# Kernel optimization log

Measured on AMD Instinct MI355X. Metric: run time of the kernel, lower is better.

## Reference

```python
import jax, jax.numpy as jnp
import numpy as np

B, S = 64, 1000
ENC, DEC = 512, 512


def setup_inputs() -> dict:
    key = jax.random.key(0)
    k1, k2, k3, k4, k5 = jax.random.split(key, 5)
    hidden = jax.random.normal(k1, (B, DEC), dtype=jnp.float32)
    encoder_outputs = jax.random.normal(k2, (B, S, 2 * ENC), dtype=jnp.float32)
    # attn: Linear(enc_hidden_dim*2 + dec_hidden_dim -> dec_hidden_dim)
    fan_in = 2 * ENC + DEC
    bound = 1.0 / np.sqrt(fan_in)
    attn_w = jax.random.uniform(k3, (fan_in, DEC), minval=-bound, maxval=bound, dtype=jnp.float32)
    attn_b = jax.random.uniform(k4, (DEC,), minval=-bound, maxval=bound, dtype=jnp.float32)
    v = jax.random.uniform(k5, (DEC,), dtype=jnp.float32)  # torch.rand -> U[0,1)
    return {"hidden": hidden, "encoder_outputs": encoder_outputs,
            "attn_w": attn_w, "attn_b": attn_b, "v": v}


def reference(hidden, encoder_outputs, attn_w, attn_b, v):
    # hidden: [B, D], encoder_outputs: [B, S, 2E]
    S_len = encoder_outputs.shape[1]
    h_rep = jnp.broadcast_to(hidden[:, None, :], (hidden.shape[0], S_len, hidden.shape[1]))
    cat = jnp.concatenate([h_rep, encoder_outputs], axis=2)          # [B, S, D+2E]
    energy = jnp.tanh(cat @ attn_w + attn_b)                          # [B, S, D]
    attention = jnp.einsum('bsd,d->bs', energy, v)                    # [B, S]
    return jax.nn.softmax(attention, axis=1)
```

## Files before the change

kernel.cpp:

```cpp
#include <hip/hip_runtime.h>
#include <hip/hip_bf16.h>

typedef __attribute__((ext_vector_type(8))) short short8;
typedef __attribute__((ext_vector_type(4))) float float4v;

__device__ inline unsigned short f2bf(float f) {
    union { float f; unsigned int i; } c; c.f = f;
    unsigned int r = c.i + 0x7FFFu + ((c.i >> 16) & 1u);
    return (unsigned short)(r >> 16);
}

__global__ void k_transpose(const float* __restrict__ W,
                            unsigned short* __restrict__ Wt) {
    int idx  = blockIdx.x * 256 + threadIdx.x;
    int lane = idx & 63;
    int nt   = (idx >> 6) & 3;
    int ks   = (idx >> 8) & 1;
    int w    = (idx >> 9) & 3;
    int c    = (idx >> 11) & 15;
    int dh   = (idx >> 15) & 1;
    int d  = dh * 256 + w * 64 + nt * 16 + (lane & 15);
    int kb = c * 64 + ks * 32 + (lane >> 4) * 8;
    short8 v;
#pragma unroll
    for (int j = 0; j < 8; j++)
        v[j] = (short)f2bf(W[(size_t)(512 + kb + j) * 512 + d]);
    *(short8*)(Wt + (size_t)idx * 8) = v;
}

__global__ void k_hb(const float* __restrict__ hidden,
                     const float* __restrict__ W,
                     const float* __restrict__ bias,
                     float* __restrict__ hb) {
    int b = blockIdx.x, d = threadIdx.x;
    __shared__ float h[512];
    h[d] = hidden[b * 512 + d];
    __syncthreads();
    float a = 0.f;
#pragma unroll 8
    for (int k = 0; k < 512; k++)
        a += h[k] * W[(size_t)k * 512 + d];
    hb[b * 512 + d] = a + bias[d];
}

__launch_bounds__(256, 3)
__global__ void k_main(const float* __restrict__ enc,
                       const unsigned short* __restrict__ Wt,
                       const float* __restrict__ hb,
                       const float* __restrict__ vvec,
                       float* __restrict__ att) {
    const int dh   = blockIdx.x;
    const int s0   = blockIdx.y * 64;
    const int b    = blockIdx.z;
    const int tid  = threadIdx.x;
    const int wave = tid >> 6;
    const int lane = tid & 63;
    const int col  = lane & 15;
    const int quad = lane >> 4;

    __shared__ unsigned short As[2][64][72];

    const int r  = tid >> 2;
    const int cq = tid & 3;
    int s = s0 + r; if (s > 999) s = 999;
    const float* arow = enc + ((size_t)(b * 1000 + s) * 1024 + cq * 16);

    const unsigned short* bbase = Wt + (size_t)dh * 262144 + wave * 4096 + lane * 8;

    float4v acc[4][4];
#pragma unroll
    for (int mt = 0; mt < 4; mt++)
#pragma unroll
        for (int nt = 0; nt < 4; nt++)
            acc[mt][nt] = float4v{0.f, 0.f, 0.f, 0.f};

    float4v st[4];
#pragma unroll
    for (int j = 0; j < 4; j++) st[j] = *(const float4v*)(arow + j * 4);
    {
        short8 wv0, wv1;
#pragma unroll
        for (int j = 0; j < 4; j++) {
            wv0[j]     = (short)f2bf(st[0][j]);
            wv0[j + 4] = (short)f2bf(st[1][j]);
            wv1[j]     = (short)f2bf(st[2][j]);
            wv1[j + 4] = (short)f2bf(st[3][j]);
        }
        unsigned short* wp = &As[0][r][cq * 16];
        *(short8*)(wp)     = wv0;
        *(short8*)(wp + 8) = wv1;
    }
    __syncthreads();

    for (int c = 0; c < 16; c++) {
        const int buf = c & 1;

        short8 bf[2][4];
#pragma unroll
        for (int ks = 0; ks < 2; ks++)
#pragma unroll
            for (int nt = 0; nt < 4; nt++)
                bf[ks][nt] = *(const short8*)(bbase + c * 16384 + (ks * 4 + nt) * 512);

        if (c < 15) {
#pragma unroll
            for (int j = 0; j < 4; j++)
                st[j] = *(const float4v*)(arow + (c + 1) * 64 + j * 4);
        }

#pragma unroll
        for (int ks = 0; ks < 2; ks++) {
            short8 af[4];
#pragma unroll
            for (int mt = 0; mt < 4; mt++)
                af[mt] = *(const short8*)(&As[buf][mt * 16 + col][ks * 32 + quad * 8]);
#pragma unroll
            for (int mt = 0; mt < 4; mt++)
#pragma unroll
                for (int nt = 0; nt < 4; nt++)
                    acc[mt][nt] = __builtin_amdgcn_mfma_f32_16x16x32_bf16(
                        af[mt], bf[ks][nt], acc[mt][nt], 0, 0, 0);
        }

        if (c < 15) {
            short8 wv0, wv1;
#pragma unroll
            for (int j = 0; j < 4; j++) {
                wv0[j]     = (short)f2bf(st[0][j]);
                wv0[j + 4] = (short)f2bf(st[1][j]);
                wv1[j]     = (short)f2bf(st[2][j]);
                wv1[j + 4] = (short)f2bf(st[3][j]);
            }
            unsigned short* wq = &As[buf ^ 1][r][cq * 16];
            *(short8*)(wq)     = wv0;
            *(short8*)(wq + 8) = wv1;
        }
        __syncthreads();
    }

    float vv[4], hbv[4];
#pragma unroll
    for (int nt = 0; nt < 4; nt++) {
        int d = dh * 256 + wave * 64 + nt * 16 + col;
        vv[nt]  = vvec[d];
        hbv[nt] = hb[b * 512 + d];
    }
    float rs[4][4];
#pragma unroll
    for (int mt = 0; mt < 4; mt++)
#pragma unroll
        for (int rg = 0; rg < 4; rg++) rs[mt][rg] = 0.f;

#pragma unroll
    for (int mt = 0; mt < 4; mt++)
#pragma unroll
        for (int nt = 0; nt < 4; nt++)
#pragma unroll
            for (int rg = 0; rg < 4; rg++) {
                float e = acc[mt][nt][rg] + hbv[nt];
                float t = 1.f - 2.f / (__expf(2.f * e) + 1.f);
                rs[mt][rg] += t * vv[nt];
            }

#pragma unroll
    for (int mt = 0; mt < 4; mt++)
#pragma unroll
        for (int rg = 0; rg < 4; rg++) {
            float x = rs[mt][rg];
            x += __shfl_xor(x, 1);
            x += __shfl_xor(x, 2);
            x += __shfl_xor(x, 4);
            x += __shfl_xor(x, 8);
            rs[mt][rg] = x;
        }

    __shared__ float red[4][64];
    if (col == 0) {
#pragma unroll
        for (int mt = 0; mt < 4; mt++)
#pragma unroll
            for (int rg = 0; rg < 4; rg++)
                red[wave][mt * 16 + quad * 4 + rg] = rs[mt][rg];
    }
    __syncthreads();
    if (tid < 64) {
        float sum = red[0][tid] + red[1][tid] + red[2][tid] + red[3][tid];
        int ss = s0 + tid;
        if (ss < 1000) att[(size_t)dh * 64000 + b * 1000 + ss] = sum;
    }
}

__global__ void k_softmax(const float* __restrict__ att,
                          float* __restrict__ out) {
    int b = blockIdx.x, tid = threadIdx.x;
    __shared__ float sm[4], ss[4];
    float x[4], mx = -1e30f;
#pragma unroll
    for (int i = 0; i < 4; i++) {
        int s = tid + 256 * i;
        if (s < 1000) {
            x[i] = att[b * 1000 + s] + att[64000 + b * 1000 + s];
        } else {
            x[i] = -1e30f;
        }
        mx = fmaxf(mx, x[i]);
    }
    for (int off = 1; off < 64; off <<= 1) mx = fmaxf(mx, __shfl_xor(mx, off));
    if ((tid & 63) == 0) sm[tid >> 6] = mx;
    __syncthreads();
    mx = fmaxf(fmaxf(sm[0], sm[1]), fmaxf(sm[2], sm[3]));

    float ex[4], se = 0.f;
#pragma unroll
    for (int i = 0; i < 4; i++) {
        ex[i] = __expf(x[i] - mx);
        if (tid + 256 * i >= 1000) ex[i] = 0.f;
        se += ex[i];
    }
    for (int off = 1; off < 64; off <<= 1) se += __shfl_xor(se, off);
    if ((tid & 63) == 0) ss[tid >> 6] = se;
    __syncthreads();
    se = ss[0] + ss[1] + ss[2] + ss[3];
    float inv = 1.f / se;
#pragma unroll
    for (int i = 0; i < 4; i++) {
        int s = tid + 256 * i;
        if (s < 1000) out[b * 1000 + s] = ex[i] * inv;
    }
}

extern "C" void kernel_launch(void* const* d_in, const int* in_sizes, int n_in,
                              void* d_out, int out_size, void* d_ws, size_t ws_size,
                              hipStream_t stream) {
    const float* hidden = (const float*)d_in[0];
    const float* enc    = (const float*)d_in[1];
    const float* attn_w = (const float*)d_in[2];
    const float* attn_b = (const float*)d_in[3];
    const float* v      = (const float*)d_in[4];
    float* out = (float*)d_out;

    char* ws = (char*)d_ws;
    unsigned short* Wt = (unsigned short*)ws;
    float* hb  = (float*)(ws + (1 << 20));
    float* att = (float*)(ws + (1 << 20) + (128 << 10));

    k_transpose<<<256, 256, 0, stream>>>(attn_w, Wt);
    k_hb<<<64, 512, 0, stream>>>(hidden, attn_w, attn_b, hb);
    k_main<<<dim3(2, 16, 64), 256, 0, stream>>>(enc, Wt, hb, v, att);
    k_softmax<<<64, 256, 0, stream>>>(att, out);
}
```

Baseline: 457.2 us.

## Stage encoder tiles via direct global-to-LDS loads and convert to bf16 at fragment read

The A-operand staging path is rewritten. Encoder rows are copied as fp32 straight from global memory into an XOR-swizzled shared buffer with global_load_lds, which bypasses registers. Conversion to bf16 now happens when fragments are read, using the packed v_cvt_pk_bf16_f32 instruction. The aim is to free registers, drop the software round-to-bf16 arithmetic, and overlap loads better. In exchange, shared memory doubles (fp32 tiles) and each tile is converted redundantly, once per reader, so occupancy could drop.

```diff
diff --git a/kernel.cpp b/kernel.cpp
--- a/kernel.cpp
+++ b/kernel.cpp
@@ -3,12 +3,27 @@
 
 typedef __attribute__((ext_vector_type(8))) short short8;
 typedef __attribute__((ext_vector_type(4))) float float4v;
+typedef __attribute__((ext_vector_type(4))) int int4v;
 
 __device__ inline unsigned short f2bf(float f) {
     union { float f; unsigned int i; } c; c.f = f;
     unsigned int r = c.i + 0x7FFFu + ((c.i >> 16) & 1u);
     return (unsigned short)(r >> 16);
 }
+
+__device__ inline short8 cvt8(float4v lo, float4v hi) {
+    int p0, p1, p2, p3;
+    asm("v_cvt_pk_bf16_f32 %0, %1, %2" : "=v"(p0) : "v"(lo[0]), "v"(lo[1]));
+    asm("v_cvt_pk_bf16_f32 %0, %1, %2" : "=v"(p1) : "v"(lo[2]), "v"(lo[3]));
+    asm("v_cvt_pk_bf16_f32 %0, %1, %2" : "=v"(p2) : "v"(hi[0]), "v"(hi[1]));
+    asm("v_cvt_pk_bf16_f32 %0, %1, %2" : "=v"(p3) : "v"(hi[2]), "v"(hi[3]));
+    int4v w; w[0] = p0; w[1] = p1; w[2] = p2; w[3] = p3;
+    union { int4v i; short8 s; } u; u.i = w;
+    return u.s;
+}
+
+typedef __attribute__((address_space(1))) const void gas_t;
+typedef __attribute__((address_space(3))) void las_t;
 
 __global__ void k_transpose(const float* __restrict__ W,
                             unsigned short* __restrict__ Wt) {
@@ -58,12 +73,23 @@
     const int col  = lane & 15;
     const int quad = lane >> 4;
 
-    __shared__ unsigned short As[2][64][72];
-
-    const int r  = tid >> 2;
-    const int cq = tid & 3;
-    int s = s0 + r; if (s > 999) s = 999;
-    const float* arow = enc + ((size_t)(b * 1000 + s) * 1024 + cq * 16);
+    __shared__ float Asf[2][64][64];
+    __shared__ float red[4][64];
+
+    const float* gbase0; const float* gbase1;
+    const float* gbase2; const float* gbase3;
+    {
+        int l4 = lane >> 4;
+#pragma unroll
+        for (int j = 0; j < 4; j++) {
+            int r = wave * 16 + j * 4 + l4;
+            int s = s0 + r; if (s > 999) s = 999;
+            int slot = (lane & 15) ^ (r & 7);
+            const float* p = enc + ((size_t)(b * 1000 + s) * 1024) + slot * 4;
+            if (j == 0) gbase0 = p; else if (j == 1) gbase1 = p;
+            else if (j == 2) gbase2 = p; else gbase3 = p;
+        }
+    }
 
     const unsigned short* bbase = Wt + (size_t)dh * 262144 + wave * 4096 + lane * 8;
 
@@ -74,22 +100,19 @@
         for (int nt = 0; nt < 4; nt++)
             acc[mt][nt] = float4v{0.f, 0.f, 0.f, 0.f};
 
-    float4v st[4];
-#pragma unroll
-    for (int j = 0; j < 4; j++) st[j] = *(const float4v*)(arow + j * 4);
-    {
-        short8 wv0, wv1;
-#pragma unroll
-        for (int j = 0; j < 4; j++) {
-            wv0[j]     = (short)f2bf(st[0][j]);
-            wv0[j + 4] = (short)f2bf(st[1][j]);
-            wv1[j]     = (short)f2bf(st[2][j]);
-            wv1[j + 4] = (short)f2bf(st[3][j]);
-        }
-        unsigned short* wp = &As[0][r][cq * 16];
-        *(short8*)(wp)     = wv0;
-        *(short8*)(wp + 8) = wv1;
-    }
+#define STAGE(nbuf, koff)                                                     \
+    do {                                                                      \
+        las_t* d0 = (las_t*)&Asf[nbuf][wave * 16 + 0][0];                     \
+        las_t* d1 = (las_t*)&Asf[nbuf][wave * 16 + 4][0];                     \
+        las_t* d2 = (las_t*)&Asf[nbuf][wave * 16 + 8][0];                     \
+        las_t* d3 = (las_t*)&Asf[nbuf][wave * 16 + 12][0];                    \
+        __builtin_amdgcn_global_load_lds((gas_t*)(gbase0 + (koff)), d0, 16, 0, 0); \
+        __builtin_amdgcn_global_load_lds((gas_t*)(gbase1 + (koff)), d1, 16, 0, 0); \
+        __builtin_amdgcn_global_load_lds((gas_t*)(gbase2 + (koff)), d2, 16, 0, 0); \
+        __builtin_amdgcn_global_load_lds((gas_t*)(gbase3 + (koff)), d3, 16, 0, 0); \
+    } while (0)
+
+    STAGE(0, 0);
     __syncthreads();
 
     for (int c = 0; c < 16; c++) {
@@ -102,41 +125,32 @@
             for (int nt = 0; nt < 4; nt++)
                 bf[ks][nt] = *(const short8*)(bbase + c * 16384 + (ks * 4 + nt) * 512);
 
-        if (c < 15) {
-#pragma unroll
-            for (int j = 0; j < 4; j++)
-                st[j] = *(const float4v*)(arow + (c + 1) * 64 + j * 4);
-        }
+        if (c < 15) STAGE(buf ^ 1, (c + 1) * 64);
 
 #pragma unroll
         for (int ks = 0; ks < 2; ks++) {
-            short8 af[4];
-#pragma unroll
-            for (int mt = 0; mt < 4; mt++)
-                af[mt] = *(const short8*)(&As[buf][mt * 16 + col][ks * 32 + quad * 8]);
-#pragma unroll
-            for (int mt = 0; mt < 4; mt++)
+            float4v r0[4], r1[4];
+#pragma unroll
+            for (int mt = 0; mt < 4; mt++) {
+                int row = mt * 16 + col;
+                int rsw = row & 7;
+                int sl0 = (ks * 8 + quad * 2 + 0) ^ rsw;
+                int sl1 = (ks * 8 + quad * 2 + 1) ^ rsw;
+                r0[mt] = *(const float4v*)(&Asf[buf][row][sl0 * 4]);
+                r1[mt] = *(const float4v*)(&Asf[buf][row][sl1 * 4]);
+            }
+#pragma unroll
+            for (int mt = 0; mt < 4; mt++) {
+                short8 af = cvt8(r0[mt], r1[mt]);
 #pragma unroll
                 for (int nt = 0; nt < 4; nt++)
                     acc[mt][nt] = __builtin_amdgcn_mfma_f32_16x16x32_bf16(
-                        af[mt], bf[ks][nt], acc[mt][nt], 0, 0, 0);
-        }
-
-        if (c < 15) {
-            short8 wv0, wv1;
-#pragma unroll
-            for (int j = 0; j < 4; j++) {
-                wv0[j]     = (short)f2bf(st[0][j]);
-                wv0[j + 4] = (short)f2bf(st[1][j]);
-                wv1[j]     = (short)f2bf(st[2][j]);
-                wv1[j + 4] = (short)f2bf(st[3][j]);
+                        af, bf[ks][nt], acc[mt][nt], 0, 0, 0);
             }
-            unsigned short* wq = &As[buf ^ 1][r][cq * 16];
-            *(short8*)(wq)     = wv0;
-            *(short8*)(wq + 8) = wv1;
         }
         __syncthreads();
     }
+#undef STAGE
 
     float vv[4], hbv[4];
 #pragma unroll
@@ -174,7 +188,6 @@
             rs[mt][rg] = x;
         }
 
-    __shared__ float red[4][64];
     if (col == 0) {
 #pragma unroll
         for (int mt = 0; mt < 4; mt++)
```

Measured after the change: 446.6 us. 2.3% less time.
